# Kernel optimization log

Hardware: AMD Instinct MI355X
Metric: run time of the kernel (lower is better)

## Reference

```python
import jax, jax.numpy as jnp
import numpy as np

B, D, H = 524288, 128, 64  # batch, input_dim, hidden_dim; mask_dim = transform_dim = D//2 = 64


def _mlp(x, Wh, bh, Wo, bo):
    """eqx.nn.MLP with depth=3: 3 hidden relu layers then linear out.
    x: [B, in]; Wh: [3, H, in/H]; bh: [3, H]; Wo: [out, H]; bo: [out]."""
    h = x
    for i in range(Wh.shape[0]):  # fixed small layer loop
        h = jax.nn.relu(h @ Wh[i].T + bh[i])
    return h @ Wo.T + bo


def setup_inputs() -> dict:
    key = jax.random.key(0)
    ks = jax.random.split(key, 9)
    m = D // 2
    s = 1.0 / np.sqrt(H)  # lecun-ish init scale
    inp = {"x": jax.random.normal(ks[0], (B, D), dtype=jnp.float32)}
    inp["cond_Wh"] = jax.random.normal(ks[1], (3, H, m), dtype=jnp.float32) * s
    inp["cond_bh"] = jnp.zeros((3, H), dtype=jnp.float32)
    inp["cond_Wo"] = jax.random.normal(ks[2], (D - m, H), dtype=jnp.float32) * s
    inp["cond_bo"] = jnp.zeros((D - m,), dtype=jnp.float32)
    inp["scale_Wh"] = jax.random.normal(ks[3], (3, H, m), dtype=jnp.float32) * s
    inp["scale_bh"] = jnp.zeros((3, H), dtype=jnp.float32)
    inp["scale_Wo"] = jax.random.normal(ks[4], (D - m, H), dtype=jnp.float32) * s
    inp["scale_bo"] = jnp.zeros((D - m,), dtype=jnp.float32)
    return inp


def reference(x, cond_Wh, cond_bh, cond_Wo, cond_bo,
              scale_Wh, scale_bh, scale_Wo, scale_bo):
    m = x.shape[-1] // 2
    # mask = [1]*m + [0]*(D-m) -> mask_idx = [:m], transform_idx = [m:] (static contiguous split)
    x_masked = x[..., :m]
    x_transform = x[..., m:]
    shift = _mlp(x_masked, cond_Wh, cond_bh, cond_Wo, cond_bo)        # [B, D-m]
    log_scale = _mlp(x_masked, scale_Wh, scale_bh, scale_Wo, scale_bo)  # [B, D-m]
    scale = jnp.exp(jnp.clip(log_scale, -5, 3))
    y_transform = x_transform * scale + shift
    y = jnp.concatenate([x_masked, y_transform], axis=-1)  # scatter back (contiguous)
    logdet = jnp.sum(log_scale, axis=-1)  # note: unclipped log_scale, as in original
    return y, logdet
```

## Files before the change

### kernel.cpp

```cpp
#include <hip/hip_runtime.h>
#include <cstdint>

typedef __attribute__((ext_vector_type(8))) _Float16 half8;
typedef __attribute__((ext_vector_type(4))) _Float16 half4;
typedef __attribute__((ext_vector_type(4))) float f32x4;

__global__ void prep_weights(const float* __restrict__ cWh, const float* __restrict__ cWo,
                             const float* __restrict__ sWh, const float* __restrict__ sWo,
                             _Float16* __restrict__ wf) {
    int t = blockIdx.x * 256 + threadIdx.x;
    int e    = t & 7;
    int mt   = (t >> 3) & 3;
    int lane = (t >> 5) & 63;
    int kp   = (t >> 11) & 1;
    int L    = (t >> 12) & 7;
    const float* src = (L < 3)  ? cWh + L * 4096
                     : (L == 3) ? cWo
                     : (L < 7)  ? sWh + (L - 4) * 4096
                     :            sWo;
    int m = mt * 16 + (lane & 15);
    int k = (2 * kp + (e >> 2)) * 16 + 4 * (lane >> 4) + (e & 3);
    float w = src[m * 64 + k];
    _Float16 hi = (_Float16)w;
    _Float16 lo = (_Float16)(w - (float)hi);
    int off = lane * 32 + mt * 8 + e;
    int fi = (L * 2 + kp) * 2;
    wf[fi * 2048 + off]       = hi;
    wf[(fi + 1) * 2048 + off] = lo;
}

template<bool RELU>
__device__ __forceinline__ half8 cvt_frag(f32x4 a, f32x4 b) {
    half8 r;
#pragma unroll
    for (int i = 0; i < 4; ++i) {
        float va = RELU ? fmaxf(a[i], 0.f) : a[i];
        float vb = RELU ? fmaxf(b[i], 0.f) : b[i];
        r[i]     = (_Float16)va;
        r[i + 4] = (_Float16)vb;
    }
    return r;
}

__device__ __forceinline__ void run_layer(const _Float16* __restrict__ wf, int Lid,
                                          const float* __restrict__ bias, int lane, int g4,
                                          const half8 B[2][4], f32x4 acc[4][4]) {
#pragma unroll
    for (int mt = 0; mt < 4; ++mt) {
        f32x4 bb = *(const f32x4*)(bias + mt * 16 + g4);
#pragma unroll
        for (int nt = 0; nt < 4; ++nt) acc[mt][nt] = bb;
    }
#pragma unroll
    for (int kp = 0; kp < 2; ++kp) {
        half8 Ah[4], Al[4];
        const _Float16* p = wf + (Lid * 2 + kp) * 4096 + lane * 32;
#pragma unroll
        for (int mt = 0; mt < 4; ++mt) {
            Ah[mt] = *(const half8*)(p + mt * 8);
            Al[mt] = *(const half8*)(p + 2048 + mt * 8);
        }
#pragma unroll
        for (int nt = 0; nt < 4; ++nt)
#pragma unroll
            for (int mt = 0; mt < 4; ++mt) {
                acc[mt][nt] = __builtin_amdgcn_mfma_f32_16x16x32_f16(Ah[mt], B[kp][nt], acc[mt][nt], 0, 0, 0);
                acc[mt][nt] = __builtin_amdgcn_mfma_f32_16x16x32_f16(Al[mt], B[kp][nt], acc[mt][nt], 0, 0, 0);
            }
    }
}

__device__ __forceinline__ void acc_to_B_relu(const f32x4 acc[4][4], half8 B[2][4]) {
#pragma unroll
    for (int kp = 0; kp < 2; ++kp)
#pragma unroll
        for (int nt = 0; nt < 4; ++nt)
            B[kp][nt] = cvt_frag<true>(acc[2 * kp][nt], acc[2 * kp + 1][nt]);
}

__global__ __launch_bounds__(64, 2)
void coupling_main(const float* __restrict__ x,
                   const float* __restrict__ cbh, const float* __restrict__ cbo,
                   const float* __restrict__ sbh, const float* __restrict__ sbo,
                   const _Float16* __restrict__ wf,
                   float* __restrict__ y, float* __restrict__ logdet) {
    const int lane = threadIdx.x;
    const int c = lane & 15;
    const int g4 = (lane >> 4) * 4;
    const long row0 = (long)blockIdx.x * 64;
    const float* xr = x + (row0 + c) * 128 + g4;
    float* yr = y + (row0 + c) * 128 + g4;

    half8 B0[2][4];
#pragma unroll
    for (int nt = 0; nt < 4; ++nt) {
        f32x4 v0 = *(const f32x4*)(xr + nt * 2048);
        f32x4 v1 = *(const f32x4*)(xr + nt * 2048 + 16);
        f32x4 v2 = *(const f32x4*)(xr + nt * 2048 + 32);
        f32x4 v3 = *(const f32x4*)(xr + nt * 2048 + 48);
        __builtin_nontemporal_store(v0, (f32x4*)(yr + nt * 2048));
        __builtin_nontemporal_store(v1, (f32x4*)(yr + nt * 2048 + 16));
        __builtin_nontemporal_store(v2, (f32x4*)(yr + nt * 2048 + 32));
        __builtin_nontemporal_store(v3, (f32x4*)(yr + nt * 2048 + 48));
        B0[0][nt] = cvt_frag<false>(v0, v1);
        B0[1][nt] = cvt_frag<false>(v2, v3);
    }

    f32x4 acc[4][4];
    half8 B[2][4];

    run_layer(wf, 0, cbh,       lane, g4, B0, acc);
    acc_to_B_relu(acc, B);
    run_layer(wf, 1, cbh + 64,  lane, g4, B, acc);
    acc_to_B_relu(acc, B);
    run_layer(wf, 2, cbh + 128, lane, g4, B, acc);
    acc_to_B_relu(acc, B);
    run_layer(wf, 3, cbo,       lane, g4, B, acc);
    half4 shp[4][4];
#pragma unroll
    for (int mt = 0; mt < 4; ++mt)
#pragma unroll
        for (int nt = 0; nt < 4; ++nt) {
            half4 s;
#pragma unroll
            for (int i = 0; i < 4; ++i) s[i] = (_Float16)acc[mt][nt][i];
            shp[mt][nt] = s;
        }

    run_layer(wf, 4, sbh,       lane, g4, B0, acc);
    acc_to_B_relu(acc, B);
    run_layer(wf, 5, sbh + 64,  lane, g4, B, acc);
    acc_to_B_relu(acc, B);
    run_layer(wf, 6, sbh + 128, lane, g4, B, acc);
    acc_to_B_relu(acc, B);
    run_layer(wf, 7, sbo,       lane, g4, B, acc);

    float pld0 = 0.f, pld1 = 0.f, pld2 = 0.f, pld3 = 0.f;
#pragma unroll
    for (int nt = 0; nt < 4; ++nt) {
        float psum = 0.f;
#pragma unroll
        for (int mt = 0; mt < 4; ++mt) {
            f32x4 ls = acc[mt][nt];
            psum += ls[0] + ls[1] + ls[2] + ls[3];
            f32x4 xt = *(const f32x4*)(xr + nt * 2048 + 64 + mt * 16);
            half4 sp = shp[mt][nt];
            f32x4 o;
#pragma unroll
            for (int i = 0; i < 4; ++i) {
                float cl = fminf(fmaxf(ls[i], -5.f), 3.f);
                o[i] = xt[i] * __expf(cl) + (float)sp[i];
            }
            __builtin_nontemporal_store(o, (f32x4*)(yr + nt * 2048 + 64 + mt * 16));
        }
        if (nt == 0) pld0 = psum; else if (nt == 1) pld1 = psum;
        else if (nt == 2) pld2 = psum; else pld3 = psum;
    }
#pragma unroll
    for (int nt = 0; nt < 4; ++nt) {
        float v = (nt == 0) ? pld0 : (nt == 1) ? pld1 : (nt == 2) ? pld2 : pld3;
        v += __shfl_xor(v, 16);
        v += __shfl_xor(v, 32);
        if ((lane >> 4) == 0) logdet[row0 + nt * 16 + c] = v;
    }
}

extern "C" void kernel_launch(void* const* d_in, const int* in_sizes, int n_in,
                              void* d_out, int out_size, void* d_ws, size_t ws_size,
                              hipStream_t stream) {
    const float* x   = (const float*)d_in[0];
    const float* cWh = (const float*)d_in[1];
    const float* cbh = (const float*)d_in[2];
    const float* cWo = (const float*)d_in[3];
    const float* cbo = (const float*)d_in[4];
    const float* sWh = (const float*)d_in[5];
    const float* sbh = (const float*)d_in[6];
    const float* sWo = (const float*)d_in[7];
    const float* sbo = (const float*)d_in[8];

    const int B = in_sizes[0] / 128;

    _Float16* wf = (_Float16*)d_ws;

    prep_weights<<<128, 256, 0, stream>>>(cWh, cWo, sWh, sWo, wf);

    float* y = (float*)d_out;
    float* logdet = y + (size_t)B * 128;
    coupling_main<<<B / 64, 64, 0, stream>>>(x, cbh, cbo, sbh, sbo, wf, y, logdet);
}
```

Before: 173.7 us.

## Stage split-fp16 weights and biases in LDS with 512-thread blocks

Packs the hi/lo fp16 weight fragments and all biases into one image, and copies that image into 130 KB of LDS at the start of each 512-thread block (8 waves of 64 rows each). Every MFMA operand load then comes from LDS instead of global/L2. The cost is a 130 KB copy per block and occupancy limited to one block per CU by the 160 KB LDS, plus a block-wide barrier before compute.

```diff
diff --git a/kernel.cpp b/kernel.cpp
--- a/kernel.cpp
+++ b/kernel.cpp
@@ -4,29 +4,38 @@
 typedef __attribute__((ext_vector_type(8))) _Float16 half8;
 typedef __attribute__((ext_vector_type(4))) _Float16 half4;
 typedef __attribute__((ext_vector_type(4))) float f32x4;
+typedef __attribute__((ext_vector_type(4))) unsigned int u32x4;
 
 __global__ void prep_weights(const float* __restrict__ cWh, const float* __restrict__ cWo,
                              const float* __restrict__ sWh, const float* __restrict__ sWo,
-                             _Float16* __restrict__ wf) {
+                             const float* __restrict__ cbh, const float* __restrict__ cbo,
+                             const float* __restrict__ sbh, const float* __restrict__ sbo,
+                             char* __restrict__ img) {
     int t = blockIdx.x * 256 + threadIdx.x;
-    int e    = t & 7;
-    int mt   = (t >> 3) & 3;
-    int lane = (t >> 5) & 63;
-    int kp   = (t >> 11) & 1;
-    int L    = (t >> 12) & 7;
-    const float* src = (L < 3)  ? cWh + L * 4096
-                     : (L == 3) ? cWo
-                     : (L < 7)  ? sWh + (L - 4) * 4096
-                     :            sWo;
-    int m = mt * 16 + (lane & 15);
-    int k = (2 * kp + (e >> 2)) * 16 + 4 * (lane >> 4) + (e & 3);
-    float w = src[m * 64 + k];
-    _Float16 hi = (_Float16)w;
-    _Float16 lo = (_Float16)(w - (float)hi);
-    int off = lane * 32 + mt * 8 + e;
-    int fi = (L * 2 + kp) * 2;
-    wf[fi * 2048 + off]       = hi;
-    wf[(fi + 1) * 2048 + off] = lo;
+    if (t < 32768) {
+        int e = t & 7, mt = (t >> 3) & 3, lane = (t >> 5) & 63, kp = (t >> 11) & 1, L = (t >> 12) & 7;
+        const float* src = (L < 3)  ? cWh + L * 4096
+                         : (L == 3) ? cWo
+                         : (L < 7)  ? sWh + (L - 4) * 4096
+                         :            sWo;
+        int m = mt * 16 + (lane & 15);
+        int k = (2 * kp + (e >> 2)) * 16 + 4 * (lane >> 4) + (e & 3);
+        float w = src[m * 64 + k];
+        _Float16 hi = (_Float16)w;
+        _Float16 lo = (_Float16)(w - (float)hi);
+        _Float16* wf = (_Float16*)img;
+        int fi = (L * 2 + kp) * 2;
+        wf[((fi * 4 + mt) * 64 + lane) * 8 + e]       = hi;
+        wf[(((fi + 1) * 4 + mt) * 64 + lane) * 8 + e] = lo;
+    } else if (t < 33280) {
+        int b = t - 32768;
+        int L = b >> 6, f = b & 63;
+        const float* src = (L < 3)  ? cbh + L * 64
+                         : (L == 3) ? cbo
+                         : (L < 7)  ? sbh + (L - 4) * 64
+                         :            sbo;
+        ((float*)(img + 131072))[b] = src[f];
+    }
 }
 
 template<bool RELU>
@@ -42,23 +51,24 @@
     return r;
 }
 
-__device__ __forceinline__ void run_layer(const _Float16* __restrict__ wf, int Lid,
-                                          const float* __restrict__ bias, int lane, int g4,
+__device__ __forceinline__ void run_layer(const _Float16* __restrict__ lwf,
+                                          const float* __restrict__ lb, int Lid,
+                                          int lane, int g4,
                                           const half8 B[2][4], f32x4 acc[4][4]) {
 #pragma unroll
     for (int mt = 0; mt < 4; ++mt) {
-        f32x4 bb = *(const f32x4*)(bias + mt * 16 + g4);
+        f32x4 bb = *(const f32x4*)(lb + Lid * 64 + mt * 16 + g4);
 #pragma unroll
         for (int nt = 0; nt < 4; ++nt) acc[mt][nt] = bb;
     }
 #pragma unroll
     for (int kp = 0; kp < 2; ++kp) {
+        const int fi = (Lid * 2 + kp) * 2;
         half8 Ah[4], Al[4];
-        const _Float16* p = wf + (Lid * 2 + kp) * 4096 + lane * 32;
 #pragma unroll
         for (int mt = 0; mt < 4; ++mt) {
-            Ah[mt] = *(const half8*)(p + mt * 8);
-            Al[mt] = *(const half8*)(p + 2048 + mt * 8);
+            Ah[mt] = *(const half8*)(lwf + ((fi * 4 + mt) * 64 + lane) * 8);
+            Al[mt] = *(const half8*)(lwf + (((fi + 1) * 4 + mt) * 64 + lane) * 8);
         }
 #pragma unroll
         for (int nt = 0; nt < 4; ++nt)
@@ -78,16 +88,24 @@
             B[kp][nt] = cvt_frag<true>(acc[2 * kp][nt], acc[2 * kp + 1][nt]);
 }
 
-__global__ __launch_bounds__(64, 2)
-void coupling_main(const float* __restrict__ x,
-                   const float* __restrict__ cbh, const float* __restrict__ cbo,
-                   const float* __restrict__ sbh, const float* __restrict__ sbo,
-                   const _Float16* __restrict__ wf,
+__global__ __launch_bounds__(512)
+void coupling_main(const float* __restrict__ x, const char* __restrict__ img,
                    float* __restrict__ y, float* __restrict__ logdet) {
-    const int lane = threadIdx.x;
+    extern __shared__ char smem[];
+    {
+        const u32x4* s = (const u32x4*)img;
+        u32x4* d = (u32x4*)smem;
+        for (int i = threadIdx.x; i < 8320; i += 512) d[i] = s[i];
+    }
+    __syncthreads();
+    const _Float16* lwf = (const _Float16*)smem;
+    const float* lb = (const float*)(smem + 131072);
+
+    const int lane = threadIdx.x & 63;
+    const int wid = threadIdx.x >> 6;
     const int c = lane & 15;
     const int g4 = (lane >> 4) * 4;
-    const long row0 = (long)blockIdx.x * 64;
+    const long row0 = (long)blockIdx.x * 512 + wid * 64;
     const float* xr = x + (row0 + c) * 128 + g4;
     float* yr = y + (row0 + c) * 128 + g4;
 
@@ -109,13 +127,13 @@
     f32x4 acc[4][4];
     half8 B[2][4];
 
-    run_layer(wf, 0, cbh,       lane, g4, B0, acc);
-    acc_to_B_relu(acc, B);
-    run_layer(wf, 1, cbh + 64,  lane, g4, B, acc);
-    acc_to_B_relu(acc, B);
-    run_layer(wf, 2, cbh + 128, lane, g4, B, acc);
-    acc_to_B_relu(acc, B);
-    run_layer(wf, 3, cbo,       lane, g4, B, acc);
+    run_layer(lwf, lb, 0, lane, g4, B0, acc);
+    acc_to_B_relu(acc, B);
+    run_layer(lwf, lb, 1, lane, g4, B, acc);
+    acc_to_B_relu(acc, B);
+    run_layer(lwf, lb, 2, lane, g4, B, acc);
+    acc_to_B_relu(acc, B);
+    run_layer(lwf, lb, 3, lane, g4, B, acc);
     half4 shp[4][4];
 #pragma unroll
     for (int mt = 0; mt < 4; ++mt)
@@ -127,13 +145,13 @@
             shp[mt][nt] = s;
         }
 
-    run_layer(wf, 4, sbh,       lane, g4, B0, acc);
-    acc_to_B_relu(acc, B);
-    run_layer(wf, 5, sbh + 64,  lane, g4, B, acc);
-    acc_to_B_relu(acc, B);
-    run_layer(wf, 6, sbh + 128, lane, g4, B, acc);
-    acc_to_B_relu(acc, B);
-    run_layer(wf, 7, sbo,       lane, g4, B, acc);
+    run_layer(lwf, lb, 4, lane, g4, B0, acc);
+    acc_to_B_relu(acc, B);
+    run_layer(lwf, lb, 5, lane, g4, B, acc);
+    acc_to_B_relu(acc, B);
+    run_layer(lwf, lb, 6, lane, g4, B, acc);
+    acc_to_B_relu(acc, B);
+    run_layer(lwf, lb, 7, lane, g4, B, acc);
 
     float pld0 = 0.f, pld1 = 0.f, pld2 = 0.f, pld3 = 0.f;
 #pragma unroll
@@ -179,12 +197,16 @@
     const float* sbo = (const float*)d_in[8];
 
     const int B = in_sizes[0] / 128;
-
-    _Float16* wf = (_Float16*)d_ws;
-
-    prep_weights<<<128, 256, 0, stream>>>(cWh, cWo, sWh, sWo, wf);
+    const int LDS_BYTES = 133120;
+
+    char* img = (char*)d_ws;
+
+    prep_weights<<<130, 256, 0, stream>>>(cWh, cWo, sWh, sWo, cbh, cbo, sbh, sbo, img);
+
+    (void)hipFuncSetAttribute((const void*)coupling_main,
+                              hipFuncAttributeMaxDynamicSharedMemorySize, LDS_BYTES);
 
     float* y = (float*)d_out;
     float* logdet = y + (size_t)B * 128;
-    coupling_main<<<B / 64, 64, 0, stream>>>(x, cbh, cbo, sbh, sbo, wf, y, logdet);
-}
+    coupling_main<<<B / 512, 512, LDS_BYTES, stream>>>(x, img, y, logdet);
+}
```

Result: slower. 177.2 us (+2.0%).
